# Performance work log

Hardware: AMD Instinct MI355X
Metric: run time of the kernel (lower is better)

The kernel has to match this reference:

```python
import jax, jax.numpy as jnp
import numpy as np

B, S, D = 2, 2048, 2048
H, KVH, DH = 16, 4, 128  # n_heads, n_kv_heads, head_dim
N_REP = H // KVH
THETA = 10000.0


def setup_inputs() -> dict:
    key = jax.random.key(0)
    ks = jax.random.split(key, 6)
    x = jax.random.normal(ks[0], (B, S, D), dtype=jnp.float32)
    wq = jax.random.normal(ks[1], (H * DH, D), dtype=jnp.float32) * (D ** -0.5)
    wk = jax.random.normal(ks[2], (KVH * DH, D), dtype=jnp.float32) * (D ** -0.5)
    wv = jax.random.normal(ks[3], (KVH * DH, D), dtype=jnp.float32) * (D ** -0.5)
    wo = jax.random.normal(ks[4], (D, H * DH), dtype=jnp.float32) * (D ** -0.5)
    # RoPE frequencies (complex freqs -> cos/sin), shape [S, DH//2]
    inv_freq = 1.0 / (THETA ** (np.arange(0, DH, 2, dtype=np.float32) / DH))
    angles = np.arange(S, dtype=np.float32)[:, None] * inv_freq[None, :]
    freqs_cos = jnp.asarray(np.cos(angles))
    freqs_sin = jnp.asarray(np.sin(angles))
    # causal additive mask [1,1,S,S]
    neg = jnp.full((S, S), -1e9, dtype=jnp.float32)
    mask = jnp.triu(neg, k=1)[None, None]
    return {"x": x, "freqs_cos": freqs_cos, "freqs_sin": freqs_sin,
            "mask": mask, "wq": wq, "wk": wk, "wv": wv, "wo": wo}


def _rope(t, cos, sin):
    # t: [B,S,h,DH]; cos/sin: [S,DH//2] -> broadcast [1,S,1,DH//2]
    tp = t.reshape(*t.shape[:-1], -1, 2)
    tr, ti = tp[..., 0], tp[..., 1]
    c = cos[None, :, None, :]
    s = sin[None, :, None, :]
    out_r = tr * c - ti * s
    out_i = tr * s + ti * c
    return jnp.stack([out_r, out_i], axis=-1).reshape(t.shape)


def reference(x, freqs_cos, freqs_sin, mask, wq, wk, wv, wo):
    b, s, _ = x.shape
    xq = jnp.einsum('bsd,ed->bse', x, wq).reshape(b, s, H, DH)
    xk = jnp.einsum('bsd,ed->bse', x, wk).reshape(b, s, KVH, DH)
    xv = jnp.einsum('bsd,ed->bse', x, wv).reshape(b, s, KVH, DH)
    xq = _rope(xq, freqs_cos, freqs_sin)
    xk = _rope(xk, freqs_cos, freqs_sin)
    # GQA: repeat kv heads
    xk = jnp.repeat(xk, N_REP, axis=2)
    xv = jnp.repeat(xv, N_REP, axis=2)
    q = xq.transpose(0, 2, 1, 3)  # [B,H,S,DH]
    k = xk.transpose(0, 2, 1, 3)
    v = xv.transpose(0, 2, 1, 3)
    scores = jnp.einsum('bhqd,bhkd->bhqk', q, k) / jnp.sqrt(jnp.float32(DH))
    scores = scores + mask
    attn = jax.nn.softmax(scores.astype(jnp.float32), axis=-1).astype(q.dtype)
    out = jnp.einsum('bhqk,bhkd->bhqd', attn, v)
    out = out.transpose(0, 2, 1, 3).reshape(b, s, H * DH)
    return jnp.einsum('bse,de->bsd', out, wo)
```

## Files before the change

kernel.cpp:

```cpp
#include <hip/hip_runtime.h>

#define Bq   2
#define Sq   2048
#define Dq   2048
#define Hq   16
#define KVHq 4
#define DHq  128

typedef unsigned short u16;
typedef short  bf16x8 __attribute__((ext_vector_type(8)));
typedef float  f32x4  __attribute__((ext_vector_type(4)));
typedef float  f32x16 __attribute__((ext_vector_type(16)));
typedef unsigned short u16x2 __attribute__((ext_vector_type(2)));
typedef unsigned short u16x4 __attribute__((ext_vector_type(4)));

__device__ __forceinline__ u16 f2bf(float f) {
    unsigned u = __float_as_uint(f);
    u += 0x7fffu + ((u >> 16) & 1u);
    return (u16)(u >> 16);
}
__device__ __forceinline__ float bf2f(u16 s) {
    return __uint_as_float(((unsigned)s) << 16);
}

__global__ void cast_bf16(const float* __restrict__ in, u16* __restrict__ out, int n4) {
    int i = blockIdx.x * 256 + threadIdx.x;
    if (i >= n4) return;
    float4 v = ((const float4*)in)[i];
    u16x4 o;
    o.x = f2bf(v.x); o.y = f2bf(v.y); o.z = f2bf(v.z); o.w = f2bf(v.w);
    ((u16x4*)out)[i] = o;
}

__global__ void cast_weights(const float* __restrict__ wq, const float* __restrict__ wk,
                             const float* __restrict__ wv, const float* __restrict__ wo,
                             u16* __restrict__ wqb, u16* __restrict__ wkvb,
                             u16* __restrict__ wob) {
    int i = blockIdx.x * 256 + threadIdx.x;
    const float4* src; u16x4* dst; int off;
    if (i < 1048576)      { src = (const float4*)wq; dst = (u16x4*)wqb;  off = i; }
    else if (i < 1310720) { src = (const float4*)wk; dst = (u16x4*)wkvb; off = i - 1048576; }
    else if (i < 1572864) { src = (const float4*)wv; dst = (u16x4*)wkvb + 262144; off = i - 1310720; }
    else                  { src = (const float4*)wo; dst = (u16x4*)wob;  off = i - 1572864; }
    float4 v = src[off];
    u16x4 o;
    o.x = f2bf(v.x); o.y = f2bf(v.y); o.z = f2bf(v.z); o.w = f2bf(v.w);
    dst[off] = o;
}

__device__ __forceinline__ void async16(const void* g, void* l) {
    __builtin_amdgcn_global_load_lds(
        (const __attribute__((address_space(1))) unsigned*)g,
        (__attribute__((address_space(3))) unsigned*)l, 16, 0, 0);
}

__device__ __forceinline__ void stc(u16* p, float v)   { *p = f2bf(v); }
__device__ __forceinline__ void stc(float* p, float v) { *p = v; }

template <typename OutT>
__global__ __launch_bounds__(256) void gemm_nt(
    const u16* __restrict__ A, const u16* __restrict__ W, OutT* __restrict__ C,
    int M, int N, int K)
{
    __shared__ __align__(16) u16 lA[128 * 32];
    __shared__ __align__(16) u16 lB[128 * 32];

    const int t    = threadIdx.x;
    const int w    = t >> 6;
    const int lane = t & 63;
    const int lr   = lane & 15;
    const int quad = lane >> 4;
    const int wm   = (w >> 1) * 64, wn = (w & 1) * 64;
    const int bm   = blockIdx.x * 128, bn = blockIdx.y * 128;

    const u16* Ab = A + (size_t)bm * K;
    const u16* Wb = W + (size_t)bn * K;

    const int r0  = t >> 2;
    const int r1  = (256 + t) >> 2;
    const int kc0 = (t & 3) * 8;

    char* la0 = (char*)lA + w * 1024;
    char* la1 = (char*)lA + 4096 + w * 1024;
    char* lb0 = (char*)lB + w * 1024;
    char* lb1 = (char*)lB + 4096 + w * 1024;

    f32x4 acc[4][4] = {};

    for (int kt = 0; kt < K; kt += 32) {
        async16(Ab + (size_t)r0 * K + kt + kc0, la0);
        async16(Ab + (size_t)r1 * K + kt + kc0, la1);
        async16(Wb + (size_t)r0 * K + kt + kc0, lb0);
        async16(Wb + (size_t)r1 * K + kt + kc0, lb1);
        __syncthreads();

        bf16x8 af[4], bfr[4];
#pragma unroll
        for (int i = 0; i < 4; i++)
            af[i] = *(const bf16x8*)&lA[(wm + i * 16 + lr) * 32 + quad * 8];
#pragma unroll
        for (int j = 0; j < 4; j++)
            bfr[j] = *(const bf16x8*)&lB[(wn + j * 16 + lr) * 32 + quad * 8];
#pragma unroll
        for (int i = 0; i < 4; i++)
#pragma unroll
            for (int j = 0; j < 4; j++)
                acc[i][j] = __builtin_amdgcn_mfma_f32_16x16x32_bf16(af[i], bfr[j], acc[i][j], 0, 0, 0);
        __syncthreads();
    }

#pragma unroll
    for (int i = 0; i < 4; i++)
#pragma unroll
        for (int j = 0; j < 4; j++)
#pragma unroll
            for (int r = 0; r < 4; r++) {
                int gm = bm + wm + i * 16 + quad * 4 + r;
                int gn = bn + wn + j * 16 + lr;
                stc(C + (size_t)gm * N + gn, acc[i][j][r]);
            }
}

__global__ void rope_k(u16* __restrict__ T, const float* __restrict__ Cs,
                       const float* __restrict__ Sn, int lognh, int total) {
    int i = blockIdx.x * 256 + threadIdx.x;
    if (i >= total) return;
    int p  = i & 63;
    int sh = i >> 6;
    int s  = (sh >> lognh) & (Sq - 1);
    float c = Cs[s * 64 + p], sn = Sn[s * 64 + p];
    u16x2* ptr = ((u16x2*)T) + i;
    u16x2 v = *ptr;
    float tr = bf2f(v.x), ti = bf2f(v.y);
    u16x2 ov;
    ov.x = f2bf(tr * c - ti * sn);
    ov.y = f2bf(tr * sn + ti * c);
    *ptr = ov;
}

__global__ void rope_kv(u16* __restrict__ KV, const float* __restrict__ Cs,
                        const float* __restrict__ Sn, int total) {
    int i = blockIdx.x * 256 + threadIdx.x;
    if (i >= total) return;
    int p     = i & 63;
    int kvh   = (i >> 6) & 3;
    int token = i >> 8;
    int s     = token & (Sq - 1);
    float c = Cs[s * 64 + p], sn = Sn[s * 64 + p];
    u16x2* ptr = ((u16x2*)KV) + (size_t)token * 512 + kvh * 64 + p;
    u16x2 v = *ptr;
    float tr = bf2f(v.x), ti = bf2f(v.y);
    u16x2 ov;
    ov.x = f2bf(tr * c - ti * sn);
    ov.y = f2bf(tr * sn + ti * c);
    *ptr = ov;
}

__global__ void transpose_v_k(const u16* __restrict__ KV, u16* __restrict__ Vt) {
    __shared__ u16 tile[32][33];
    const int bk = blockIdx.z;
    const int b = bk >> 2, kvh = bk & 3;
    const int s0 = blockIdx.x * 32, d0 = blockIdx.y * 32;
    const int tx = threadIdx.x, ty = threadIdx.y;
    tile[ty][tx] = KV[(size_t)(b * Sq + s0 + ty) * 1024 + 512 + kvh * 128 + d0 + tx];
    __syncthreads();
    Vt[((size_t)bk * DHq + d0 + ty) * Sq + s0 + tx] = tile[tx][ty];
}

#define PSCALE 0.12753102f
#define PBIAS  17.31234049f

__global__ __launch_bounds__(256, 2) void flash_attn_sk2(
    const u16* __restrict__ Q, const u16* __restrict__ KV,
    const u16* __restrict__ Vt, float* __restrict__ Oc, float* __restrict__ Lc)
{
    __shared__ __align__(16) u16 kl[4 * 64 * 32];
    __shared__ __align__(16) u16 vl[2 * 128 * 32];
    __shared__ __align__(16) u16 pl[4][32 * 72];

    const int bh = blockIdx.x;
    const int b = bh >> 4, h = bh & 15;
    const int kvh = h >> 2;
    const int c = blockIdx.y;
    int qt, ci, nc;
    if (c < 4)       { qt = c;                    ci = 0;            nc = 1; }
    else if (c < 12) { qt = 4  + ((c - 4) >> 1);  ci = (c - 4) & 1;  nc = 2; }
    else if (c < 24) { qt = 8  + (c - 12) / 3;    ci = (c - 12) % 3; nc = 3; }
    else             { qt = 12 + ((c - 24) >> 2); ci = (c - 24) & 3; nc = 4; }
    const int T  = 2 * (qt + 1);
    const int t0 = (ci * T) / nc, t1 = ((ci + 1) * T) / nc;

    const int tid = threadIdx.x;
    const int w = tid >> 6, lane = tid & 63;
    const int col = lane & 31, hi = lane >> 5;
    const int q0 = qt * 128 + w * 32;

    const u16* Qp = Q + (size_t)(b * Sq + q0 + col) * (Hq * DHq) + h * DHq + hi * 8;
    bf16x8 qf[8];
#pragma unroll
    for (int ks = 0; ks < 8; ks++) qf[ks] = *(const bf16x8*)(Qp + ks * 16);

    const u16* Kg = KV + (size_t)b * Sq * 1024 + kvh * DHq;
    const u16* Vg = Vt + (size_t)(b * KVHq + kvh) * DHq * Sq;

    const int srow = lane >> 2;
    const int sc   = (lane & 3) * 8;

    f32x16 o[4] = {};
    float lsum[16] = {};

    for (int kt = t0; kt < t1; kt++) {
        const int kb = kt * 64;
#pragma unroll
        for (int c4 = 0; c4 < 4; c4++) {
            const u16* g = Kg + (size_t)(kb + w * 16 + srow) * 1024 + c4 * 32 + sc;
            async16(g, (char*)kl + (c4 * 2048 + w * 512) * 2 + lane * 16);
        }
#pragma unroll
        for (int c4 = 0; c4 < 4; c4++) {
            const int g2 = c4 & 1, dbase = (c4 >> 1) * 64;
            const u16* g = Vg + (size_t)(dbase + w * 16 + srow) * Sq + kb + g2 * 32 + sc;
            async16(g, (char*)vl + (g2 * 4096 + (dbase + w * 16) * 32) * 2 + lane * 16);
        }
        __syncthreads();

        f32x16 s0 = {}, s1 = {};
#pragma unroll
        for (int ks = 0; ks < 8; ks++) {
            const int kkbase = (ks >> 1) * 2048 + (ks & 1) * 16 + hi * 8;
            bf16x8 k0 = *(const bf16x8*)&kl[kkbase + col * 32];
            bf16x8 k1 = *(const bf16x8*)&kl[kkbase + (32 + col) * 32];
            s0 = __builtin_amdgcn_mfma_f32_32x32x16_bf16(qf[ks], k0, s0, 0, 0, 0);
            s1 = __builtin_amdgcn_mfma_f32_32x32x16_bf16(qf[ks], k1, s1, 0, 0, 0);
        }

#pragma unroll
        for (int r = 0; r < 16; r++) {
            const int rloc = (r & 3) + 8 * (r >> 2) + 4 * hi;
            const int qg = q0 + rloc;
            float v0 = s0[r] * PSCALE - PBIAS;
            float v1 = s1[r] * PSCALE - PBIAS;
            float p0 = (kb + col      <= qg) ? exp2f(v0) : 0.f;
            float p1 = (kb + 32 + col <= qg) ? exp2f(v1) : 0.f;
            lsum[r] += p0 + p1;
            pl[w][rloc * 72 + col]      = f2bf(p0);
            pl[w][rloc * 72 + 32 + col] = f2bf(p1);
        }

#pragma unroll
        for (int ks = 0; ks < 4; ks++) {
            bf16x8 pa = *(const bf16x8*)&pl[w][col * 72 + ks * 16 + hi * 8];
            const int vbase = (ks >> 1) * 4096 + (ks & 1) * 16 + hi * 8;
#pragma unroll
            for (int n = 0; n < 4; n++) {
                bf16x8 vf = *(const bf16x8*)&vl[vbase + (n * 32 + col) * 32];
                o[n] = __builtin_amdgcn_mfma_f32_32x32x16_bf16(pa, vf, o[n], 0, 0, 0);
            }
        }
        __syncthreads();
    }

    float* Ocb = Oc + (size_t)(bh * 40 + c) * 16384 + (size_t)w * 32 * 128;
    float* Lcb = Lc + (size_t)(bh * 40 + c) * 128 + w * 32;
#pragma unroll
    for (int r = 0; r < 16; r++) {
        const int rloc = (r & 3) + 8 * (r >> 2) + 4 * hi;
        float t = lsum[r];
        t += __shfl_xor(t, 1);
        t += __shfl_xor(t, 2);
        t += __shfl_xor(t, 4);
        t += __shfl_xor(t, 8);
        t += __shfl_xor(t, 16);
        if (col == 0) Lcb[rloc] = t;
#pragma unroll
        for (int n = 0; n < 4; n++)
            Ocb[rloc * 128 + n * 32 + col] = o[n][r];
    }
}

__global__ __launch_bounds__(256) void flash_reduce2(
    const float* __restrict__ Oc, const float* __restrict__ Lc, u16* __restrict__ AO)
{
    const int bh = blockIdx.x;
    const int qt = blockIdx.y;
    const int e  = blockIdx.z * 256 + threadIdx.x;
    const int row = e >> 5, col4 = e & 31;
    int cst, nc;
    if (qt < 4)       { cst = qt;                 nc = 1; }
    else if (qt < 8)  { cst = 4  + 2 * (qt - 4);  nc = 2; }
    else if (qt < 12) { cst = 12 + 3 * (qt - 8);  nc = 3; }
    else              { cst = 24 + 4 * (qt - 12); nc = 4; }
    f32x4 acc = {0.f, 0.f, 0.f, 0.f};
    float l = 0.f;
    for (int i = 0; i < nc; i++) {
        const size_t base = (size_t)(bh * 40 + cst + i);
        acc += ((const f32x4*)(Oc + base * 16384))[e];
        l   += Lc[base * 128 + row];
    }
    const float inv = 1.0f / l;
    const int b = bh >> 4, h = bh & 15;
    u16x4 ov;
    ov.x = f2bf(acc[0] * inv); ov.y = f2bf(acc[1] * inv);
    ov.z = f2bf(acc[2] * inv); ov.w = f2bf(acc[3] * inv);
    u16* dst = AO + (size_t)(b * Sq + qt * 128 + row) * (Hq * DHq) + h * DHq + col4 * 4;
    *(u16x4*)dst = ov;
}

__global__ __launch_bounds__(256) void flash_attn(
    const u16* __restrict__ Q, const u16* __restrict__ KV,
    const u16* __restrict__ Vt, u16* __restrict__ O)
{
    __shared__ __align__(16) u16 plds[4][16 * 72];
    const int bh = blockIdx.x;
    const int b = bh >> 4, h = bh & 15;
    const int kvh = h >> 2;
    const int w = threadIdx.x >> 6, lane = threadIdx.x & 63;
    const int lr = lane & 15, quad = lane >> 4;
    const int yy = gridDim.y - 1 - blockIdx.y;
    const int q0 = yy * 64 + w * 16;

    const u16* Qp = Q + (size_t)(b * Sq + q0 + lr) * (Hq * DHq) + h * DHq + quad * 8;
    bf16x8 qf[4];
#pragma unroll
    for (int kk = 0; kk < 4; kk++) qf[kk] = *(const bf16x8*)(Qp + kk * 32);

    const u16* Kp = KV + (size_t)b * Sq * 1024 + kvh * DHq;
    const u16* Vp = Vt + (size_t)(b * KVHq + kvh) * DHq * Sq;

    f32x4 o[8] = {};
    float lsum[4] = {0.f, 0.f, 0.f, 0.f};

    const int nt = (q0 + 16 + 63) >> 6;
    for (int kt = 0; kt < nt; kt++) {
        const int kb = kt * 64;
        f32x4 s[4] = {};
#pragma unroll
        for (int kk = 0; kk < 4; kk++) {
#pragma unroll
            for (int j = 0; j < 4; j++) {
                bf16x8 kf = *(const bf16x8*)(Kp + (size_t)(kb + j * 16 + lr) * 1024 + kk * 32 + quad * 8);
                s[j] = __builtin_amdgcn_mfma_f32_16x16x32_bf16(qf[kk], kf, s[j], 0, 0, 0);
            }
        }
#pragma unroll
        for (int r = 0; r < 4; r++) {
            const int qg = q0 + quad * 4 + r;
#pragma unroll
            for (int j = 0; j < 4; j++) {
                float v = s[j][r] * PSCALE - PBIAS;
                float p = (kb + j * 16 + lr <= qg) ? exp2f(v) : 0.f;
                lsum[r] += p;
                plds[w][(quad * 4 + r) * 72 + j * 16 + lr] = f2bf(p);
            }
        }
        bf16x8 pa0 = *(const bf16x8*)&plds[w][lr * 72 + quad * 8];
        bf16x8 pa1 = *(const bf16x8*)&plds[w][lr * 72 + 32 + quad * 8];
#pragma unroll
        for (int dt = 0; dt < 8; dt++) {
            bf16x8 v0 = *(const bf16x8*)(Vp + (size_t)(dt * 16 + lr) * Sq + kb + quad * 8);
            bf16x8 v1 = *(const bf16x8*)(Vp + (size_t)(dt * 16 + lr) * Sq + kb + 32 + quad * 8);
            o[dt] = __builtin_amdgcn_mfma_f32_16x16x32_bf16(pa0, v0, o[dt], 0, 0, 0);
            o[dt] = __builtin_amdgcn_mfma_f32_16x16x32_bf16(pa1, v1, o[dt], 0, 0, 0);
        }
    }

    u16* Ob = O + (size_t)(b * Sq) * (Hq * DHq) + h * DHq;
#pragma unroll
    for (int r = 0; r < 4; r++) {
        float t = lsum[r];
        t += __shfl_xor(t, 1);
        t += __shfl_xor(t, 2);
        t += __shfl_xor(t, 4);
        t += __shfl_xor(t, 8);
        const float inv = 1.0f / t;
        const int qg = q0 + quad * 4 + r;
#pragma unroll
        for (int dt = 0; dt < 8; dt++)
            Ob[(size_t)qg * (Hq * DHq) + dt * 16 + lr] = f2bf(o[dt][r] * inv);
    }
}

extern "C" void kernel_launch(void* const* d_in, const int* in_sizes, int n_in,
                              void* d_out, int out_size, void* d_ws, size_t ws_size,
                              hipStream_t stream) {
    const float* x  = (const float*)d_in[0];
    const float* fc = (const float*)d_in[1];
    const float* fs = (const float*)d_in[2];
    const float* wq = (const float*)d_in[4];
    const float* wk = (const float*)d_in[5];
    const float* wv = (const float*)d_in[6];
    const float* wo = (const float*)d_in[7];
    float* out = (float*)d_out;

    char* ws = (char*)d_ws;
    u16* xb   = (u16*)(ws);
    u16* wqb  = (u16*)(ws + 16777216);
    u16* wkvb = (u16*)(ws + 25165824);
    u16* wob  = (u16*)(ws + 29360128);
    u16* Qb   = (u16*)(ws + 37748736);
    u16* KVb  = (u16*)(ws + 54525952);
    u16* Vtb  = (u16*)(ws + 62914560);
    u16* AOb  = (u16*)(ws + 67108864);
    float* Ocb = (float*)(ws + 83886080);
    float* Lcb = (float*)(ws + 167772160);
    const size_t WS_NEED = 168427520;

    cast_bf16<<<8192, 256, 0, stream>>>(x, xb, 2097152);
    cast_weights<<<10240, 256, 0, stream>>>(wq, wk, wv, wo, wqb, wkvb, wob);

    dim3 blk(256);
    gemm_nt<u16><<<dim3(32, 16), blk, 0, stream>>>(xb, wqb,  Qb,  4096, 2048, 2048);
    gemm_nt<u16><<<dim3(32, 8),  blk, 0, stream>>>(xb, wkvb, KVb, 4096, 1024, 2048);

    rope_k<<<16384, 256, 0, stream>>>(Qb, fc, fs, 4, 4194304);
    rope_kv<<<4096, 256, 0, stream>>>(KVb, fc, fs, 1048576);

    transpose_v_k<<<dim3(64, 4, 8), dim3(32, 32), 0, stream>>>(KVb, Vtb);

    if (ws_size >= WS_NEED) {
        flash_attn_sk2<<<dim3(32, 40), blk, 0, stream>>>(Qb, KVb, Vtb, Ocb, Lcb);
        flash_reduce2<<<dim3(32, 16, 16), blk, 0, stream>>>(Ocb, Lcb, AOb);
    } else {
        flash_attn<<<dim3(32, 32), blk, 0, stream>>>(Qb, KVb, Vtb, AOb);
    }

    gemm_nt<float><<<dim3(32, 16), blk, 0, stream>>>(AOb, wob, out, 4096, 2048, 2048);
}
```

Baseline: 404.4 us.

## Fuse Q/KV projections into one QKV GEMM and swizzle flash-attn LDS layout

Concatenates the Q, K and V weight matrices so a single GEMM produces an interleaved QKV buffer, and drops the separate KV GEMM launch. The two RoPE kernels are merged into one parameterised kernel, and the attention kernels read through the new 3072-wide row stride. The flash attention K/V LDS tiles get an XOR swizzle meant to cut bank conflicts, and launch bounds are raised to allow 3 blocks per CU. The wider row stride makes Q/K loads less contiguous, and the higher occupancy target could force register spills.

```diff
diff --git a/kernel.cpp b/kernel.cpp
--- a/kernel.cpp
+++ b/kernel.cpp
@@ -34,14 +34,13 @@
 
 __global__ void cast_weights(const float* __restrict__ wq, const float* __restrict__ wk,
                              const float* __restrict__ wv, const float* __restrict__ wo,
-                             u16* __restrict__ wqb, u16* __restrict__ wkvb,
-                             u16* __restrict__ wob) {
+                             u16* __restrict__ wqkvb, u16* __restrict__ wob) {
     int i = blockIdx.x * 256 + threadIdx.x;
     const float4* src; u16x4* dst; int off;
-    if (i < 1048576)      { src = (const float4*)wq; dst = (u16x4*)wqb;  off = i; }
-    else if (i < 1310720) { src = (const float4*)wk; dst = (u16x4*)wkvb; off = i - 1048576; }
-    else if (i < 1572864) { src = (const float4*)wv; dst = (u16x4*)wkvb + 262144; off = i - 1310720; }
-    else                  { src = (const float4*)wo; dst = (u16x4*)wob;  off = i - 1572864; }
+    if (i < 1048576)      { src = (const float4*)wq; dst = (u16x4*)wqkvb; off = i; }
+    else if (i < 1310720) { src = (const float4*)wk; dst = (u16x4*)wqkvb + 1048576; off = i - 1048576; }
+    else if (i < 1572864) { src = (const float4*)wv; dst = (u16x4*)wqkvb + 1310720; off = i - 1310720; }
+    else                  { src = (const float4*)wo; dst = (u16x4*)wob; off = i - 1572864; }
     float4 v = src[off];
     u16x4 o;
     o.x = f2bf(v.x); o.y = f2bf(v.y); o.z = f2bf(v.z); o.w = f2bf(v.w);
@@ -121,15 +120,16 @@
             }
 }
 
-__global__ void rope_k(u16* __restrict__ T, const float* __restrict__ Cs,
-                       const float* __restrict__ Sn, int lognh, int total) {
+__global__ void rope_qk(u16* __restrict__ T, const float* __restrict__ Cs,
+                        const float* __restrict__ Sn, int lognh, int base, int total) {
     int i = blockIdx.x * 256 + threadIdx.x;
     if (i >= total) return;
-    int p  = i & 63;
-    int sh = i >> 6;
-    int s  = (sh >> lognh) & (Sq - 1);
+    int p     = i & 63;
+    int h     = (i >> 6) & ((1 << lognh) - 1);
+    int token = i >> (6 + lognh);
+    int s     = token & (Sq - 1);
     float c = Cs[s * 64 + p], sn = Sn[s * 64 + p];
-    u16x2* ptr = ((u16x2*)T) + i;
+    u16x2* ptr = (u16x2*)T + (size_t)token * 1536 + base + h * 64 + p;
     u16x2 v = *ptr;
     float tr = bf2f(v.x), ti = bf2f(v.y);
     u16x2 ov;
@@ -138,31 +138,13 @@
     *ptr = ov;
 }
 
-__global__ void rope_kv(u16* __restrict__ KV, const float* __restrict__ Cs,
-                        const float* __restrict__ Sn, int total) {
-    int i = blockIdx.x * 256 + threadIdx.x;
-    if (i >= total) return;
-    int p     = i & 63;
-    int kvh   = (i >> 6) & 3;
-    int token = i >> 8;
-    int s     = token & (Sq - 1);
-    float c = Cs[s * 64 + p], sn = Sn[s * 64 + p];
-    u16x2* ptr = ((u16x2*)KV) + (size_t)token * 512 + kvh * 64 + p;
-    u16x2 v = *ptr;
-    float tr = bf2f(v.x), ti = bf2f(v.y);
-    u16x2 ov;
-    ov.x = f2bf(tr * c - ti * sn);
-    ov.y = f2bf(tr * sn + ti * c);
-    *ptr = ov;
-}
-
-__global__ void transpose_v_k(const u16* __restrict__ KV, u16* __restrict__ Vt) {
+__global__ void transpose_v_k(const u16* __restrict__ QKV, u16* __restrict__ Vt) {
     __shared__ u16 tile[32][33];
     const int bk = blockIdx.z;
     const int b = bk >> 2, kvh = bk & 3;
     const int s0 = blockIdx.x * 32, d0 = blockIdx.y * 32;
     const int tx = threadIdx.x, ty = threadIdx.y;
-    tile[ty][tx] = KV[(size_t)(b * Sq + s0 + ty) * 1024 + 512 + kvh * 128 + d0 + tx];
+    tile[ty][tx] = QKV[(size_t)(b * Sq + s0 + ty) * 3072 + 2560 + kvh * 128 + d0 + tx];
     __syncthreads();
     Vt[((size_t)bk * DHq + d0 + ty) * Sq + s0 + tx] = tile[tx][ty];
 }
@@ -170,9 +152,9 @@
 #define PSCALE 0.12753102f
 #define PBIAS  17.31234049f
 
-__global__ __launch_bounds__(256, 2) void flash_attn_sk2(
-    const u16* __restrict__ Q, const u16* __restrict__ KV,
-    const u16* __restrict__ Vt, float* __restrict__ Oc, float* __restrict__ Lc)
+__global__ __launch_bounds__(256, 3) void flash_attn_sk2(
+    const u16* __restrict__ QKV, const u16* __restrict__ Vt,
+    float* __restrict__ Oc, float* __restrict__ Lc)
 {
     __shared__ __align__(16) u16 kl[4 * 64 * 32];
     __shared__ __align__(16) u16 vl[2 * 128 * 32];
@@ -193,18 +175,19 @@
     const int tid = threadIdx.x;
     const int w = tid >> 6, lane = tid & 63;
     const int col = lane & 31, hi = lane >> 5;
+    const int sw = (col >> 1) & 3;
     const int q0 = qt * 128 + w * 32;
 
-    const u16* Qp = Q + (size_t)(b * Sq + q0 + col) * (Hq * DHq) + h * DHq + hi * 8;
+    const u16* Qp = QKV + (size_t)(b * Sq + q0 + col) * 3072 + h * 128 + hi * 8;
     bf16x8 qf[8];
 #pragma unroll
     for (int ks = 0; ks < 8; ks++) qf[ks] = *(const bf16x8*)(Qp + ks * 16);
 
-    const u16* Kg = KV + (size_t)b * Sq * 1024 + kvh * DHq;
+    const u16* Kg = QKV + (size_t)b * Sq * 3072 + 2048 + kvh * 128;
     const u16* Vg = Vt + (size_t)(b * KVHq + kvh) * DHq * Sq;
 
     const int srow = lane >> 2;
-    const int sc   = (lane & 3) * 8;
+    const int swc  = ((lane & 3) ^ ((lane >> 3) & 3)) * 8;
 
     f32x16 o[4] = {};
     float lsum[16] = {};
@@ -213,23 +196,24 @@
         const int kb = kt * 64;
 #pragma unroll
         for (int c4 = 0; c4 < 4; c4++) {
-            const u16* g = Kg + (size_t)(kb + w * 16 + srow) * 1024 + c4 * 32 + sc;
-            async16(g, (char*)kl + (c4 * 2048 + w * 512) * 2 + lane * 16);
+            const u16* g = Kg + (size_t)(kb + w * 16 + srow) * 3072 + c4 * 32 + swc;
+            async16(g, (char*)kl + c4 * 4096 + w * 1024 + lane * 16);
         }
 #pragma unroll
         for (int c4 = 0; c4 < 4; c4++) {
             const int g2 = c4 & 1, dbase = (c4 >> 1) * 64;
-            const u16* g = Vg + (size_t)(dbase + w * 16 + srow) * Sq + kb + g2 * 32 + sc;
-            async16(g, (char*)vl + (g2 * 4096 + (dbase + w * 16) * 32) * 2 + lane * 16);
+            const u16* g = Vg + (size_t)(dbase + w * 16 + srow) * Sq + kb + g2 * 32 + swc;
+            async16(g, (char*)vl + g2 * 8192 + (dbase + w * 16) * 64 + lane * 16);
         }
         __syncthreads();
 
         f32x16 s0 = {}, s1 = {};
 #pragma unroll
         for (int ks = 0; ks < 8; ks++) {
-            const int kkbase = (ks >> 1) * 2048 + (ks & 1) * 16 + hi * 8;
-            bf16x8 k0 = *(const bf16x8*)&kl[kkbase + col * 32];
-            bf16x8 k1 = *(const bf16x8*)&kl[kkbase + (32 + col) * 32];
+            const int j = (((ks & 1) * 2 + hi) ^ sw) & 3;
+            const int base = (ks >> 1) * 2048 + j * 8;
+            bf16x8 k0 = *(const bf16x8*)&kl[base + col * 32];
+            bf16x8 k1 = *(const bf16x8*)&kl[base + (32 + col) * 32];
             s0 = __builtin_amdgcn_mfma_f32_32x32x16_bf16(qf[ks], k0, s0, 0, 0, 0);
             s1 = __builtin_amdgcn_mfma_f32_32x32x16_bf16(qf[ks], k1, s1, 0, 0, 0);
         }
@@ -250,7 +234,8 @@
 #pragma unroll
         for (int ks = 0; ks < 4; ks++) {
             bf16x8 pa = *(const bf16x8*)&pl[w][col * 72 + ks * 16 + hi * 8];
-            const int vbase = (ks >> 1) * 4096 + (ks & 1) * 16 + hi * 8;
+            const int j = (((ks & 1) * 2 + hi) ^ sw) & 3;
+            const int vbase = (ks >> 1) * 4096 + j * 8;
 #pragma unroll
             for (int n = 0; n < 4; n++) {
                 bf16x8 vf = *(const bf16x8*)&vl[vbase + (n * 32 + col) * 32];
@@ -307,8 +292,7 @@
 }
 
 __global__ __launch_bounds__(256) void flash_attn(
-    const u16* __restrict__ Q, const u16* __restrict__ KV,
-    const u16* __restrict__ Vt, u16* __restrict__ O)
+    const u16* __restrict__ QKV, const u16* __restrict__ Vt, u16* __restrict__ O)
 {
     __shared__ __align__(16) u16 plds[4][16 * 72];
     const int bh = blockIdx.x;
@@ -319,12 +303,12 @@
     const int yy = gridDim.y - 1 - blockIdx.y;
     const int q0 = yy * 64 + w * 16;
 
-    const u16* Qp = Q + (size_t)(b * Sq + q0 + lr) * (Hq * DHq) + h * DHq + quad * 8;
+    const u16* Qp = QKV + (size_t)(b * Sq + q0 + lr) * 3072 + h * 128 + quad * 8;
     bf16x8 qf[4];
 #pragma unroll
     for (int kk = 0; kk < 4; kk++) qf[kk] = *(const bf16x8*)(Qp + kk * 32);
 
-    const u16* Kp = KV + (size_t)b * Sq * 1024 + kvh * DHq;
+    const u16* Kp = QKV + (size_t)b * Sq * 3072 + 2048 + kvh * 128;
     const u16* Vp = Vt + (size_t)(b * KVHq + kvh) * DHq * Sq;
 
     f32x4 o[8] = {};
@@ -338,7 +322,7 @@
         for (int kk = 0; kk < 4; kk++) {
 #pragma unroll
             for (int j = 0; j < 4; j++) {
-                bf16x8 kf = *(const bf16x8*)(Kp + (size_t)(kb + j * 16 + lr) * 1024 + kk * 32 + quad * 8);
+                bf16x8 kf = *(const bf16x8*)(Kp + (size_t)(kb + j * 16 + lr) * 3072 + kk * 32 + quad * 8);
                 s[j] = __builtin_amdgcn_mfma_f32_16x16x32_bf16(qf[kk], kf, s[j], 0, 0, 0);
             }
         }
@@ -393,35 +377,32 @@
     float* out = (float*)d_out;
 
     char* ws = (char*)d_ws;
-    u16* xb   = (u16*)(ws);
-    u16* wqb  = (u16*)(ws + 16777216);
-    u16* wkvb = (u16*)(ws + 25165824);
-    u16* wob  = (u16*)(ws + 29360128);
-    u16* Qb   = (u16*)(ws + 37748736);
-    u16* KVb  = (u16*)(ws + 54525952);
-    u16* Vtb  = (u16*)(ws + 62914560);
-    u16* AOb  = (u16*)(ws + 67108864);
+    u16* xb    = (u16*)(ws);
+    u16* wqkvb = (u16*)(ws + 16777216);
+    u16* wob   = (u16*)(ws + 29360128);
+    u16* QKVb  = (u16*)(ws + 37748736);
+    u16* Vtb   = (u16*)(ws + 62914560);
+    u16* AOb   = (u16*)(ws + 67108864);
     float* Ocb = (float*)(ws + 83886080);
     float* Lcb = (float*)(ws + 167772160);
     const size_t WS_NEED = 168427520;
 
     cast_bf16<<<8192, 256, 0, stream>>>(x, xb, 2097152);
-    cast_weights<<<10240, 256, 0, stream>>>(wq, wk, wv, wo, wqb, wkvb, wob);
+    cast_weights<<<10240, 256, 0, stream>>>(wq, wk, wv, wo, wqkvb, wob);
 
     dim3 blk(256);
-    gemm_nt<u16><<<dim3(32, 16), blk, 0, stream>>>(xb, wqb,  Qb,  4096, 2048, 2048);
-    gemm_nt<u16><<<dim3(32, 8),  blk, 0, stream>>>(xb, wkvb, KVb, 4096, 1024, 2048);
-
-    rope_k<<<16384, 256, 0, stream>>>(Qb, fc, fs, 4, 4194304);
-    rope_kv<<<4096, 256, 0, stream>>>(KVb, fc, fs, 1048576);
-
-    transpose_v_k<<<dim3(64, 4, 8), dim3(32, 32), 0, stream>>>(KVb, Vtb);
+    gemm_nt<u16><<<dim3(32, 24), blk, 0, stream>>>(xb, wqkvb, QKVb, 4096, 3072, 2048);
+
+    rope_qk<<<16384, 256, 0, stream>>>(QKVb, fc, fs, 4, 0,    4194304);
+    rope_qk<<<4096,  256, 0, stream>>>(QKVb, fc, fs, 2, 1024, 1048576);
+
+    transpose_v_k<<<dim3(64, 4, 8), dim3(32, 32), 0, stream>>>(QKVb, Vtb);
 
     if (ws_size >= WS_NEED) {
-        flash_attn_sk2<<<dim3(32, 40), blk, 0, stream>>>(Qb, KVb, Vtb, Ocb, Lcb);
+        flash_attn_sk2<<<dim3(32, 40), blk, 0, stream>>>(QKVb, Vtb, Ocb, Lcb);
         flash_reduce2<<<dim3(32, 16, 16), blk, 0, stream>>>(Ocb, Lcb, AOb);
     } else {
-        flash_attn<<<dim3(32, 32), blk, 0, stream>>>(Qb, KVb, Vtb, AOb);
+        flash_attn<<<dim3(32, 32), blk, 0, stream>>>(QKVb, Vtb, AOb);
     }
 
     gemm_nt<float><<<dim3(32, 16), blk, 0, stream>>>(AOb, wob, out, 4096, 2048, 2048);
```

Measured after the change: 528.0 us. +30.6%, slower.
